# Optimization experiments

Hardware: AMD Instinct MI355X
Metric: run time of the kernel (lower is better)

Reference implementation:

```python
import jax, jax.numpy as jnp
import numpy as np
import math

SHAPES = [(64, 64), (32, 32), (16, 16), (8, 8)]  # (H_l, W_l), sum HW = 5440
N, LQ, D, NH, NL, NP = 4, 5440, 256, 8, 4, 4
HD = D // NH


def _offset_bias():
    thetas = np.arange(NH, dtype=np.float64) * (2.0 * math.pi / NH)
    grid = np.stack([np.cos(thetas), np.sin(thetas)], -1)
    grid = grid / np.abs(grid).max(-1, keepdims=True)
    grid = np.tile(grid[:, None, None, :], (1, NL, NP, 1))
    grid = grid * (np.arange(NP) + 1)[None, None, :, None]
    return jnp.asarray(grid.reshape(-1), jnp.float32)


def setup_inputs() -> dict:
    key = jax.random.key(0)
    ks = jax.random.split(key, 16)
    s = 1.0 / math.sqrt(D)
    inp = {
        'query0': jax.random.normal(ks[0], (N, LQ, D), jnp.float32),
        'query1': jax.random.normal(ks[1], (N, LQ, D), jnp.float32),
        'feat0': jax.random.normal(ks[2], (N, LQ, D), jnp.float32),
        'feat1': jax.random.normal(ks[3], (N, LQ, D), jnp.float32),
        'reference_points': jax.random.uniform(ks[4], (N, LQ, NL, 2), jnp.float32),
        'W_off': 0.01 * jax.random.normal(ks[5], (NH * NL * NP * 2, D), jnp.float32),
        'b_off': _offset_bias(),
        'W_attn': 0.01 * jax.random.normal(ks[6], (NH * NL * NP, D), jnp.float32),
        'b_attn': jnp.zeros((NH * NL * NP,), jnp.float32),
        'W_val': s * jax.random.normal(ks[7], (D, D), jnp.float32),
        'b_val': jnp.zeros((D,), jnp.float32),
        'W_out': s * jax.random.normal(ks[8], (D, D), jnp.float32),
        'b_out': jnp.zeros((D,), jnp.float32),
        'W_agg': s * jax.random.normal(ks[9], (D, 2 * D), jnp.float32),
        'b_agg': jnp.zeros((D,), jnp.float32),
    }
    return inp


def _sample_level(value_l, H, W, loc):
    # value_l: (N, H*W, NH, HD); loc: (N, LQ, NH, NP, 2) normalized in [0,1]
    v_t = value_l.transpose(0, 2, 1, 3)  # (N, NH, HW, HD)
    # grid_sample bilinear, align_corners=False, zero padding:
    x = loc[..., 0] * W - 0.5
    y = loc[..., 1] * H - 0.5
    x0 = jnp.floor(x); y0 = jnp.floor(y)
    lx = x - x0; ly = y - y0
    x0 = x0.astype(jnp.int32); y0 = y0.astype(jnp.int32)

    def corner(xi, yi, w):
        valid = (xi >= 0) & (xi < W) & (yi >= 0) & (yi < H)
        flat = jnp.clip(yi, 0, H - 1) * W + jnp.clip(xi, 0, W - 1)  # (N,LQ,NH,NP)
        ft = flat.transpose(0, 2, 1, 3).reshape(flat.shape[0], flat.shape[2], -1)
        g = jnp.take_along_axis(v_t, ft[..., None], axis=2)  # (N,NH,LQ*NP,HD)
        g = g.reshape(v_t.shape[0], v_t.shape[1], loc.shape[1], loc.shape[3], -1)
        g = g.transpose(0, 2, 1, 3, 4)  # (N,LQ,NH,NP,HD)
        return g * (w * valid)[..., None]

    return (corner(x0, y0, (1 - lx) * (1 - ly)) + corner(x0 + 1, y0, lx * (1 - ly))
            + corner(x0, y0 + 1, (1 - lx) * ly) + corner(x0 + 1, y0 + 1, lx * ly))


def reference(query0, query1, feat0, feat1, reference_points, W_off, b_off,
              W_attn, b_attn, W_val, b_val, W_out, b_out, W_agg, b_agg):
    offset_norm = jnp.asarray([[w, h] for (h, w) in SHAPES], jnp.float32)  # (NL, 2)
    sizes = [h * w for h, w in SHAPES]
    splits = list(np.cumsum(sizes)[:-1])
    outs = []
    for q, feat in ((query0, feat0), (query1, feat1)):
        value = (feat @ W_val.T + b_val).reshape(N, -1, NH, HD)
        off = (q @ W_off.T + b_off).reshape(N, LQ, NH, NL, NP, 2)
        attn = (q @ W_attn.T + b_attn).reshape(N, LQ, NH, NL * NP)
        attn = jax.nn.softmax(attn, axis=-1).reshape(N, LQ, NH, NL, NP)
        loc = reference_points[:, :, None, :, None, :] + off / offset_norm[None, None, None, :, None, :]
        vals = jnp.split(value, splits, axis=1)
        acc = jnp.zeros((N, LQ, NH, HD), value.dtype)
        for l, (H, W) in enumerate(SHAPES):
            s = _sample_level(vals[l], H, W, loc[:, :, :, l])  # (N,LQ,NH,NP,HD)
            acc = acc + jnp.einsum('nqhpd,nqhp->nqhd', s, attn[:, :, :, l])
        outs.append(acc.reshape(N, LQ, D) @ W_out.T + b_out)
    return jnp.concatenate(outs, axis=-1) @ W_agg.T + b_agg
```

## Files before the change

### kernel.cpp

```cpp
#include <hip/hip_runtime.h>
#include <math.h>

#define N_   4
#define LQ_  5440
#define MQ_  (N_*LQ_)

typedef _Float16 f16;
typedef __attribute__((ext_vector_type(2))) _Float16 f16x2;
typedef __attribute__((ext_vector_type(8))) _Float16 f16x8;
typedef __attribute__((ext_vector_type(4))) float     f32x4;

__device__ __forceinline__ unsigned short f2h(float f) {
  union { f16 h; unsigned short u; } v; v.h = (f16)f; return v.u;
}
__device__ __forceinline__ float h2f(unsigned u) {
  union { unsigned short u; f16 h; } v; v.u = (unsigned short)u; return (float)v.h;
}
__device__ __forceinline__ f16x2 u2h2(unsigned u) {
  union { unsigned u; f16x2 h; } v; v.u = u; return v.h;
}

#define GLD16(gp, lp) __builtin_amdgcn_global_load_lds( \
    (const __attribute__((address_space(1))) void*)(gp), \
    (__attribute__((address_space(3))) void*)(lp), 16, 0, 0)

__global__ __launch_bounds__(256)
void prep(const float* __restrict__ W_val, const float* __restrict__ W_off,
          const float* __restrict__ W_attn, const float* __restrict__ W_agg,
          const float* __restrict__ W_out, const float* __restrict__ b_off,
          const float* __restrict__ b_attn, const float* __restrict__ b_agg,
          const float* __restrict__ b_out,
          unsigned short* __restrict__ Wvalh, unsigned short* __restrict__ Wcath,
          unsigned short* __restrict__ Wfinh, float* __restrict__ bcat,
          float* __restrict__ bfin) {
  __shared__ float wrow[256];
  const int b = blockIdx.x, t = threadIdx.x;
  if (b < 160) {
    const float* src; unsigned short* dst; int i;
    if (b < 64)       { src = W_val;  dst = Wvalh;          i = b * 256 + t; }
    else if (b < 128) { src = W_off;  dst = Wcath;          i = (b - 64) * 256 + t; }
    else              { src = W_attn; dst = Wcath + 65536;  i = (b - 128) * 256 + t; }
    float4 v = reinterpret_cast<const float4*>(src)[i];
    ushort4 r;
    r.x = f2h(v.x); r.y = f2h(v.y); r.z = f2h(v.z); r.w = f2h(v.w);
    reinterpret_cast<ushort4*>(dst)[i] = r;
  } else if (b < 672) {
    const int idx = b - 160, j = idx & 255, s = idx >> 8;
    wrow[t] = W_agg[(size_t)j * 512 + s * 256 + t];
    __syncthreads();
    float a = 0.f;
    for (int i = 0; i < 256; ++i) a = fmaf(wrow[i], W_out[(size_t)i * 256 + t], a);
    Wfinh[(size_t)j * 512 + s * 256 + t] = f2h(a);
  } else if (b == 672) {
    float s = b_agg[t];
    for (int i = 0; i < 256; ++i)
      s = fmaf(W_agg[(size_t)t * 512 + i] + W_agg[(size_t)t * 512 + 256 + i], b_out[i], s);
    bfin[t] = s;
  } else if (b == 673) {
    bcat[t] = b_off[t];
  } else {
    if (t < 128) bcat[256 + t] = b_attn[t];
  }
}

__global__ __launch_bounds__(256)
void gemm_stage1(const float* __restrict__ q0, const float* __restrict__ q1,
                 const float* __restrict__ f0, const float* __restrict__ f1,
                 const unsigned short* __restrict__ Wvalh,
                 const unsigned short* __restrict__ Wcath,
                 const float* __restrict__ b_val, const float* __restrict__ bcat,
                 unsigned short* __restrict__ valb, unsigned short* __restrict__ oab) {
  __shared__ __align__(16) unsigned short As[128 * 64];
  __shared__ __align__(16) unsigned short Ws[128 * 64];
  const int src = blockIdx.y, z = blockIdx.z;
  const size_t SZ = (size_t)MQ_ * 256;
  const float* A; const unsigned short* W; const float* bias;
  unsigned short* C; int NC, NT;
  if (src == 0) { A = z ? f1 : f0; W = Wvalh; bias = b_val; C = valb + z * SZ;               NC = 256; NT = 2; }
  else          { A = z ? q1 : q0; W = Wcath; bias = bcat;  C = oab + (size_t)z * MQ_ * 384; NC = 384; NT = 3; }

  const int t    = threadIdx.x;
  const int lane = t & 63;
  const int wv   = t >> 6;
  const int wr   = wv >> 1, wc = wv & 1;
  const int row0 = blockIdx.x * 128;
  const int srow = t >> 3, schunk = t & 7;
  const int wbase = wv * 512;

  for (int ct = 0; ct < NT; ++ct) {
    const int col0 = ct * 128;
    f32x4 acc[4][4] = {};

    for (int k0 = 0; k0 < 256; k0 += 64) {
      __syncthreads();
      #pragma unroll
      for (int i = 0; i < 4; ++i) {
        const int row = i * 32 + srow;
        const int ch  = schunk ^ (row & 7);
        GLD16(W + (size_t)(col0 + row) * 256 + k0 + ch * 8, &Ws[i * 2048 + wbase]);
      }
      #pragma unroll
      for (int i = 0; i < 4; ++i) {
        const int row = i * 32 + srow;
        const float* srcp = A + (size_t)(row0 + row) * 256 + k0 + schunk * 8;
        const float4 a0 = *reinterpret_cast<const float4*>(srcp);
        const float4 a1 = *reinterpret_cast<const float4*>(srcp + 4);
        f16x8 hv;
        hv[0] = (f16)a0.x; hv[1] = (f16)a0.y; hv[2] = (f16)a0.z; hv[3] = (f16)a0.w;
        hv[4] = (f16)a1.x; hv[5] = (f16)a1.y; hv[6] = (f16)a1.z; hv[7] = (f16)a1.w;
        const int ch = schunk ^ (row & 7);
        *reinterpret_cast<f16x8*>(&As[row * 64 + ch * 8]) = hv;
      }
      __syncthreads();

      f16x8 af[4][2], bfr[4][2];
      #pragma unroll
      for (int f = 0; f < 4; ++f)
        #pragma unroll
        for (int kk = 0; kk < 2; ++kk) {
          const int ra = wr * 64 + f * 16 + (lane & 15);
          const int ca = (kk * 4 + (lane >> 4)) ^ (ra & 7);
          af[f][kk] = *(const f16x8*)&As[ra * 64 + ca * 8];
          const int rb = wc * 64 + f * 16 + (lane & 15);
          const int cb = (kk * 4 + (lane >> 4)) ^ (rb & 7);
          bfr[f][kk] = *(const f16x8*)&Ws[rb * 64 + cb * 8];
        }
      #pragma unroll
      for (int kk = 0; kk < 2; ++kk)
        #pragma unroll
        for (int fm = 0; fm < 4; ++fm)
          #pragma unroll
          for (int fn = 0; fn < 4; ++fn)
            acc[fm][fn] = __builtin_amdgcn_mfma_f32_16x16x32_f16(
                af[fm][kk], bfr[fn][kk], acc[fm][fn], 0, 0, 0);
    }

    #pragma unroll
    for (int fm = 0; fm < 4; ++fm) {
      const int m = row0 + wr * 64 + fm * 16 + (lane >> 4) * 4;
      #pragma unroll
      for (int fn = 0; fn < 4; ++fn) {
        const int c = col0 + wc * 64 + fn * 16 + (lane & 15);
        const float bv = bias[c];
        #pragma unroll
        for (int r = 0; r < 4; ++r)
          C[(size_t)(m + r) * NC + c] = f2h(acc[fm][fn][r] + bv);
      }
    }
  }
}

__global__ __launch_bounds__(256)
void gemm_final(const unsigned short* __restrict__ A,
                const unsigned short* __restrict__ W,
                const float* __restrict__ bias, float* __restrict__ out) {
  __shared__ __align__(16) unsigned short As[64 * 64];
  __shared__ __align__(16) unsigned short Ws[128 * 64];
  const int t    = threadIdx.x;
  const int lane = t & 63;
  const int wv   = t >> 6;
  const int row0 = blockIdx.x * 64, col0 = blockIdx.y * 128;
  const int srow = t >> 3, schunk = t & 7;
  const int wbase = wv * 512;

  f32x4 acc[4][2] = {};

  for (int k0 = 0; k0 < 512; k0 += 64) {
    __syncthreads();
    #pragma unroll
    for (int i = 0; i < 2; ++i) {
      const int row = i * 32 + srow;
      const int ch  = schunk ^ (row & 7);
      GLD16(A + (size_t)(row0 + row) * 512 + k0 + ch * 8, &As[i * 2048 + wbase]);
    }
    #pragma unroll
    for (int i = 0; i < 4; ++i) {
      const int row = i * 32 + srow;
      const int ch  = schunk ^ (row & 7);
      GLD16(W + (size_t)(col0 + row) * 512 + k0 + ch * 8, &Ws[i * 2048 + wbase]);
    }
    __syncthreads();

    f16x8 af[4][2], bfr[2][2];
    #pragma unroll
    for (int kk = 0; kk < 2; ++kk) {
      #pragma unroll
      for (int f = 0; f < 4; ++f) {
        const int ra = f * 16 + (lane & 15);
        const int ca = (kk * 4 + (lane >> 4)) ^ (ra & 7);
        af[f][kk] = *(const f16x8*)&As[ra * 64 + ca * 8];
      }
      #pragma unroll
      for (int fn = 0; fn < 2; ++fn) {
        const int rb = wv * 32 + fn * 16 + (lane & 15);
        const int cb = (kk * 4 + (lane >> 4)) ^ (rb & 7);
        bfr[fn][kk] = *(const f16x8*)&Ws[rb * 64 + cb * 8];
      }
    }
    #pragma unroll
    for (int kk = 0; kk < 2; ++kk)
      #pragma unroll
      for (int fm = 0; fm < 4; ++fm)
        #pragma unroll
        for (int fn = 0; fn < 2; ++fn)
          acc[fm][fn] = __builtin_amdgcn_mfma_f32_16x16x32_f16(
              af[fm][kk], bfr[fn][kk], acc[fm][fn], 0, 0, 0);
  }

  #pragma unroll
  for (int fm = 0; fm < 4; ++fm) {
    const int m = row0 + fm * 16 + (lane >> 4) * 4;
    #pragma unroll
    for (int fn = 0; fn < 2; ++fn) {
      const int c = col0 + wv * 32 + fn * 16 + (lane & 15);
      const float bv = bias[c];
      #pragma unroll
      for (int r = 0; r < 4; ++r)
        out[(size_t)(m + r) * 256 + c] = acc[fm][fn][r] + bv;
    }
  }
}

__global__ __launch_bounds__(256, 4)
void deform_sample(const unsigned short* __restrict__ vals,
                   const unsigned short* __restrict__ oa,
                   const float* __restrict__ refp,
                   unsigned short* __restrict__ acc_out) {
  const int bid = blockIdx.x;
  const int sn  = bid & 7;
  const int s   = sn >> 2, n = sn & 3;
  const int qb  = bid >> 3;
  const int t   = threadIdx.x;
  const int q   = t >> 5, tq = t & 31;
  const int row = n * LQ_ + qb * 8 + q;
  const int h   = tq >> 2;
  __shared__ uint4 lds_rec[8][16][8];

  const unsigned short* oar = oa + ((size_t)s * MQ_ + row) * 384;
  {
    const int   l  = tq & 3;
    const int   Wn = 64 >> l;
    const float Wf = (float)Wn;
    const int   lb = (int)(((0xAD200u >> (5 * l)) & 31u) << 8);
    const uint4 ov = *reinterpret_cast<const uint4*>(oar + (size_t)tq * 8);
    const uint2 lv = *reinterpret_cast<const uint2*>(oar + 256 + (size_t)tq * 4);
    const float2 rxy = *reinterpret_cast<const float2*>(refp + (size_t)row * 8 + l * 2);
    float lg[4] = { h2f(lv.x), h2f(lv.x >> 16), h2f(lv.y), h2f(lv.y >> 16) };
    float mx = fmaxf(fmaxf(lg[0], lg[1]), fmaxf(lg[2], lg[3]));
    mx = fmaxf(mx, __shfl_xor(mx, 1));
    mx = fmaxf(mx, __shfl_xor(mx, 2));
    float e[4], se;
    #pragma unroll
    for (int k = 0; k < 4; ++k) e[k] = __expf(lg[k] - mx);
    se = (e[0] + e[1]) + (e[2] + e[3]);
    se += __shfl_xor(se, 1);
    se += __shfl_xor(se, 2);
    const float inv = 1.f / se;
    const unsigned od[4] = { ov.x, ov.y, ov.z, ov.w };
    #pragma unroll
    for (int k = 0; k < 4; ++k) {
      const float ox = h2f(od[k]), oy = h2f(od[k] >> 16);
      const float x = fmaf(rxy.x, Wf, ox) - 0.5f;
      const float y = fmaf(rxy.y, Wf, oy) - 0.5f;
      const float x0f = floorf(x), y0f = floorf(y);
      const int   x0 = (int)x0f,   y0 = (int)y0f;
      const float lx = x - x0f,    ly = y - y0f;
      const float aw = e[k] * inv;
      const int   xs[2] = {x0, x0 + 1}, ys[2] = {y0, y0 + 1};
      const float wx[2] = {1.f - lx, lx}, wy[2] = {1.f - ly, ly};
      unsigned ia[4]; unsigned short wa[4];
      #pragma unroll
      for (int cy = 0; cy < 2; ++cy)
        #pragma unroll
        for (int cx = 0; cx < 2; ++cx) {
          const int xi = xs[cx], yi = ys[cy];
          const bool v = (xi >= 0) && (xi < Wn) && (yi >= 0) && (yi < Wn);
          const int xc = min(max(xi, 0), Wn - 1), yc = min(max(yi, 0), Wn - 1);
          ia[cy * 2 + cx] = (unsigned)(lb + yc * Wn + xc);
          wa[cy * 2 + cx] = f2h(v ? wx[cx] * wy[cy] * aw : 0.f);
        }
      const int jj = l * 4 + k;
      uint4 rec;
      rec.x = ia[0] | (ia[1] << 16);
      rec.y = ia[2] | (ia[3] << 16);
      rec.z = (unsigned)wa[0] | ((unsigned)wa[1] << 16);
      rec.w = (unsigned)wa[2] | ((unsigned)wa[3] << 16);
      lds_rec[q][jj][h ^ (jj & 7)] = rec;
    }
  }
  __syncthreads();

  const int dg = tq & 3;
  const char* vb = (const char*)(vals + ((size_t)s * N_ + n) * LQ_ * 256);
  const unsigned hd = (unsigned)((h * 32 + dg * 8) * 2);
  float facc[8] = {};
  #pragma unroll 1
  for (int l4 = 0; l4 < 4; ++l4) {
    uint4 m[4];
    #pragma unroll
    for (int p = 0; p < 4; ++p) {
      const int j = l4 * 4 + p;
      m[p] = lds_rec[q][j][h ^ (j & 7)];
    }
    f16x8 v[16];
    #pragma unroll
    for (int p = 0; p < 4; ++p) {
      v[p * 4 + 0] = *reinterpret_cast<const f16x8*>(vb + (((m[p].x & 0xffffu) << 9) + hd));
      v[p * 4 + 1] = *reinterpret_cast<const f16x8*>(vb + (((m[p].x >> 16) << 9) + hd));
      v[p * 4 + 2] = *reinterpret_cast<const f16x8*>(vb + (((m[p].y & 0xffffu) << 9) + hd));
      v[p * 4 + 3] = *reinterpret_cast<const f16x8*>(vb + (((m[p].y >> 16) << 9) + hd));
    }
    __builtin_amdgcn_sched_barrier(0);
    f16x2 a0 = {0, 0}, a1 = {0, 0}, a2 = {0, 0}, a3 = {0, 0};
    #pragma unroll
    for (int p = 0; p < 4; ++p) {
      const f16x2 w0 = u2h2(__builtin_amdgcn_perm(m[p].z, m[p].z, 0x01000100u));
      const f16x2 w1 = u2h2(__builtin_amdgcn_perm(m[p].z, m[p].z, 0x03020302u));
      const f16x2 w2 = u2h2(__builtin_amdgcn_perm(m[p].w, m[p].w, 0x01000100u));
      const f16x2 w3 = u2h2(__builtin_amdgcn_perm(m[p].w, m[p].w, 0x03020302u));
      const f16x2* p0 = (const f16x2*)&v[p * 4 + 0];
      const f16x2* p1 = (const f16x2*)&v[p * 4 + 1];
      const f16x2* p2 = (const f16x2*)&v[p * 4 + 2];
      const f16x2* p3 = (const f16x2*)&v[p * 4 + 3];
      a0 = __builtin_elementwise_fma(p0[0], w0, a0);
      a1 = __builtin_elementwise_fma(p0[1], w0, a1);
      a2 = __builtin_elementwise_fma(p0[2], w0, a2);
      a3 = __builtin_elementwise_fma(p0[3], w0, a3);
      a0 = __builtin_elementwise_fma(p1[0], w1, a0);
      a1 = __builtin_elementwise_fma(p1[1], w1, a1);
      a2 = __builtin_elementwise_fma(p1[2], w1, a2);
      a3 = __builtin_elementwise_fma(p1[3], w1, a3);
      a0 = __builtin_elementwise_fma(p2[0], w2, a0);
      a1 = __builtin_elementwise_fma(p2[1], w2, a1);
      a2 = __builtin_elementwise_fma(p2[2], w2, a2);
      a3 = __builtin_elementwise_fma(p2[3], w2, a3);
      a0 = __builtin_elementwise_fma(p3[0], w3, a0);
      a1 = __builtin_elementwise_fma(p3[1], w3, a1);
      a2 = __builtin_elementwise_fma(p3[2], w3, a2);
      a3 = __builtin_elementwise_fma(p3[3], w3, a3);
    }
    facc[0] += (float)a0[0]; facc[1] += (float)a0[1];
    facc[2] += (float)a1[0]; facc[3] += (float)a1[1];
    facc[4] += (float)a2[0]; facc[5] += (float)a2[1];
    facc[6] += (float)a3[0]; facc[7] += (float)a3[1];
  }
  f16x8 r;
  #pragma unroll
  for (int e2 = 0; e2 < 8; ++e2) r[e2] = (f16)facc[e2];
  *reinterpret_cast<f16x8*>(acc_out + (size_t)row * 512 + s * 256 + h * 32 + dg * 8) = r;
}

extern "C" void kernel_launch(void* const* d_in, const int* in_sizes, int n_in,
                              void* d_out, int out_size, void* d_ws, size_t ws_size,
                              hipStream_t stream) {
  const float* query0 = (const float*)d_in[0];
  const float* query1 = (const float*)d_in[1];
  const float* feat0  = (const float*)d_in[2];
  const float* feat1  = (const float*)d_in[3];
  const float* refp   = (const float*)d_in[4];
  const float* W_off  = (const float*)d_in[5];
  const float* b_off  = (const float*)d_in[6];
  const float* W_attn = (const float*)d_in[7];
  const float* b_attn = (const float*)d_in[8];
  const float* W_val  = (const float*)d_in[9];
  const float* b_val  = (const float*)d_in[10];
  const float* W_out  = (const float*)d_in[11];
  const float* b_out  = (const float*)d_in[12];
  const float* W_agg  = (const float*)d_in[13];
  const float* b_agg  = (const float*)d_in[14];
  float* out = (float*)d_out;

  char* p = (char*)d_ws;
  const size_t SZ = (size_t)MQ_ * 256;
  unsigned short* valb  = (unsigned short*)p; p += 2 * SZ * 2;
  unsigned short* oab   = (unsigned short*)p; p += (size_t)2 * MQ_ * 384 * 2;
  unsigned short* accb  = (unsigned short*)p; p += (size_t)MQ_ * 512 * 2;
  unsigned short* Wvalh = (unsigned short*)p; p += 256 * 256 * 2;
  unsigned short* Wcath = (unsigned short*)p; p += 384 * 256 * 2;
  unsigned short* Wfinh = (unsigned short*)p; p += 256 * 512 * 2;
  float* bcat = (float*)p; p += 384 * 4;
  float* bfin = (float*)p; p += 256 * 4;

  prep<<<675, 256, 0, stream>>>(W_val, W_off, W_attn, W_agg, W_out, b_off, b_attn,
                                b_agg, b_out, Wvalh, Wcath, Wfinh, bcat, bfin);
  gemm_stage1<<<dim3(170, 2, 2), 256, 0, stream>>>(query0, query1, feat0, feat1,
                                                   Wvalh, Wcath, b_val, bcat,
                                                   valb, oab);
  deform_sample<<<5440, 256, 0, stream>>>(valb, oab, refp, accb);
  gemm_final<<<dim3(340, 2), 256, 0, stream>>>(accb, Wfinh, bfin, out);
}
```

Baseline: 137.1 us.

## Remove prep kernel by converting weights inline and folding W_out into sampler

The separate prep launch goes away. gemm_stage1 now reads the fp32 W_val, W_off and W_attn directly and converts them to fp16 while staging into LDS, replacing the async global_load_lds copy of pre-converted weights, and it reads the bias arrays directly. The W_agg·W_out fusion and the final bias computation become 513 extra blocks appended to the deform_sample grid, which removes one kernel launch and its serialization gap. In exchange, the GEMM does redundant fp32 weight loads and conversions in every block, and the extra tail blocks in the sampler are compute-serial.

```diff
diff --git a/kernel.cpp b/kernel.cpp
--- a/kernel.cpp
+++ b/kernel.cpp
@@ -25,59 +25,20 @@
     (__attribute__((address_space(3))) void*)(lp), 16, 0, 0)
 
 __global__ __launch_bounds__(256)
-void prep(const float* __restrict__ W_val, const float* __restrict__ W_off,
-          const float* __restrict__ W_attn, const float* __restrict__ W_agg,
-          const float* __restrict__ W_out, const float* __restrict__ b_off,
-          const float* __restrict__ b_attn, const float* __restrict__ b_agg,
-          const float* __restrict__ b_out,
-          unsigned short* __restrict__ Wvalh, unsigned short* __restrict__ Wcath,
-          unsigned short* __restrict__ Wfinh, float* __restrict__ bcat,
-          float* __restrict__ bfin) {
-  __shared__ float wrow[256];
-  const int b = blockIdx.x, t = threadIdx.x;
-  if (b < 160) {
-    const float* src; unsigned short* dst; int i;
-    if (b < 64)       { src = W_val;  dst = Wvalh;          i = b * 256 + t; }
-    else if (b < 128) { src = W_off;  dst = Wcath;          i = (b - 64) * 256 + t; }
-    else              { src = W_attn; dst = Wcath + 65536;  i = (b - 128) * 256 + t; }
-    float4 v = reinterpret_cast<const float4*>(src)[i];
-    ushort4 r;
-    r.x = f2h(v.x); r.y = f2h(v.y); r.z = f2h(v.z); r.w = f2h(v.w);
-    reinterpret_cast<ushort4*>(dst)[i] = r;
-  } else if (b < 672) {
-    const int idx = b - 160, j = idx & 255, s = idx >> 8;
-    wrow[t] = W_agg[(size_t)j * 512 + s * 256 + t];
-    __syncthreads();
-    float a = 0.f;
-    for (int i = 0; i < 256; ++i) a = fmaf(wrow[i], W_out[(size_t)i * 256 + t], a);
-    Wfinh[(size_t)j * 512 + s * 256 + t] = f2h(a);
-  } else if (b == 672) {
-    float s = b_agg[t];
-    for (int i = 0; i < 256; ++i)
-      s = fmaf(W_agg[(size_t)t * 512 + i] + W_agg[(size_t)t * 512 + 256 + i], b_out[i], s);
-    bfin[t] = s;
-  } else if (b == 673) {
-    bcat[t] = b_off[t];
-  } else {
-    if (t < 128) bcat[256 + t] = b_attn[t];
-  }
-}
-
-__global__ __launch_bounds__(256)
 void gemm_stage1(const float* __restrict__ q0, const float* __restrict__ q1,
                  const float* __restrict__ f0, const float* __restrict__ f1,
-                 const unsigned short* __restrict__ Wvalh,
-                 const unsigned short* __restrict__ Wcath,
-                 const float* __restrict__ b_val, const float* __restrict__ bcat,
+                 const float* __restrict__ Wval32, const float* __restrict__ Woff32,
+                 const float* __restrict__ Wattn32,
+                 const float* __restrict__ b_val, const float* __restrict__ b_off,
+                 const float* __restrict__ b_attn,
                  unsigned short* __restrict__ valb, unsigned short* __restrict__ oab) {
   __shared__ __align__(16) unsigned short As[128 * 64];
   __shared__ __align__(16) unsigned short Ws[128 * 64];
   const int src = blockIdx.y, z = blockIdx.z;
   const size_t SZ = (size_t)MQ_ * 256;
-  const float* A; const unsigned short* W; const float* bias;
-  unsigned short* C; int NC, NT;
-  if (src == 0) { A = z ? f1 : f0; W = Wvalh; bias = b_val; C = valb + z * SZ;               NC = 256; NT = 2; }
-  else          { A = z ? q1 : q0; W = Wcath; bias = bcat;  C = oab + (size_t)z * MQ_ * 384; NC = 384; NT = 3; }
+  const float* A; unsigned short* C; int NC, NT;
+  if (src == 0) { A = z ? f1 : f0; C = valb + z * SZ;               NC = 256; NT = 2; }
+  else          { A = z ? q1 : q0; C = oab + (size_t)z * MQ_ * 384; NC = 384; NT = 3; }
 
   const int t    = threadIdx.x;
   const int lane = t & 63;
@@ -85,10 +46,14 @@
   const int wr   = wv >> 1, wc = wv & 1;
   const int row0 = blockIdx.x * 128;
   const int srow = t >> 3, schunk = t & 7;
-  const int wbase = wv * 512;
 
   for (int ct = 0; ct < NT; ++ct) {
     const int col0 = ct * 128;
+    const float* Wsrc; const float* bias; int wrow0;
+    if (src == 0)      { Wsrc = Wval32;  bias = b_val  + col0; wrow0 = col0; }
+    else if (ct < 2)   { Wsrc = Woff32;  bias = b_off  + col0; wrow0 = col0; }
+    else               { Wsrc = Wattn32; bias = b_attn;        wrow0 = 0;    }
+
     f32x4 acc[4][4] = {};
 
     for (int k0 = 0; k0 < 256; k0 += 64) {
@@ -96,8 +61,14 @@
       #pragma unroll
       for (int i = 0; i < 4; ++i) {
         const int row = i * 32 + srow;
-        const int ch  = schunk ^ (row & 7);
-        GLD16(W + (size_t)(col0 + row) * 256 + k0 + ch * 8, &Ws[i * 2048 + wbase]);
+        const float* wp = Wsrc + (size_t)(wrow0 + row) * 256 + k0 + schunk * 8;
+        const float4 w0 = *reinterpret_cast<const float4*>(wp);
+        const float4 w1 = *reinterpret_cast<const float4*>(wp + 4);
+        f16x8 hw;
+        hw[0] = (f16)w0.x; hw[1] = (f16)w0.y; hw[2] = (f16)w0.z; hw[3] = (f16)w0.w;
+        hw[4] = (f16)w1.x; hw[5] = (f16)w1.y; hw[6] = (f16)w1.z; hw[7] = (f16)w1.w;
+        const int ch = schunk ^ (row & 7);
+        *reinterpret_cast<f16x8*>(&Ws[row * 64 + ch * 8]) = hw;
       }
       #pragma unroll
       for (int i = 0; i < 4; ++i) {
@@ -140,11 +111,11 @@
       const int m = row0 + wr * 64 + fm * 16 + (lane >> 4) * 4;
       #pragma unroll
       for (int fn = 0; fn < 4; ++fn) {
-        const int c = col0 + wc * 64 + fn * 16 + (lane & 15);
-        const float bv = bias[c];
+        const int cl = wc * 64 + fn * 16 + (lane & 15);
+        const float bv = bias[cl];
         #pragma unroll
         for (int r = 0; r < 4; ++r)
-          C[(size_t)(m + r) * NC + c] = f2h(acc[fm][fn][r] + bv);
+          C[(size_t)(m + r) * NC + col0 + cl] = f2h(acc[fm][fn][r] + bv);
       }
     }
   }
@@ -225,16 +196,41 @@
 void deform_sample(const unsigned short* __restrict__ vals,
                    const unsigned short* __restrict__ oa,
                    const float* __restrict__ refp,
-                   unsigned short* __restrict__ acc_out) {
+                   unsigned short* __restrict__ acc_out,
+                   const float* __restrict__ W_agg, const float* __restrict__ W_out,
+                   const float* __restrict__ b_agg, const float* __restrict__ b_out,
+                   unsigned short* __restrict__ Wfinh, float* __restrict__ bfin) {
+  __shared__ uint4 lds_rec[8][16][8];
   const int bid = blockIdx.x;
+  const int t   = threadIdx.x;
+
+  if (bid >= 5440) {
+    const int pb = bid - 5440;
+    float* wrow = (float*)lds_rec;
+    if (pb < 512) {
+      const int j = pb & 255, s2 = pb >> 8;
+      wrow[t] = W_agg[(size_t)j * 512 + s2 * 256 + t];
+      __syncthreads();
+      float a = 0.f;
+      for (int i = 0; i < 256; ++i)
+        a = fmaf(wrow[i], W_out[(size_t)i * 256 + t], a);
+      Wfinh[(size_t)j * 512 + s2 * 256 + t] = f2h(a);
+    } else {
+      float s2 = b_agg[t];
+      for (int i = 0; i < 256; ++i)
+        s2 = fmaf(W_agg[(size_t)t * 512 + i] + W_agg[(size_t)t * 512 + 256 + i],
+                  b_out[i], s2);
+      bfin[t] = s2;
+    }
+    return;
+  }
+
   const int sn  = bid & 7;
   const int s   = sn >> 2, n = sn & 3;
   const int qb  = bid >> 3;
-  const int t   = threadIdx.x;
   const int q   = t >> 5, tq = t & 31;
   const int row = n * LQ_ + qb * 8 + q;
   const int h   = tq >> 2;
-  __shared__ uint4 lds_rec[8][16][8];
 
   const unsigned short* oar = oa + ((size_t)s * MQ_ + row) * 384;
   {
@@ -375,17 +371,15 @@
   unsigned short* valb  = (unsigned short*)p; p += 2 * SZ * 2;
   unsigned short* oab   = (unsigned short*)p; p += (size_t)2 * MQ_ * 384 * 2;
   unsigned short* accb  = (unsigned short*)p; p += (size_t)MQ_ * 512 * 2;
-  unsigned short* Wvalh = (unsigned short*)p; p += 256 * 256 * 2;
-  unsigned short* Wcath = (unsigned short*)p; p += 384 * 256 * 2;
   unsigned short* Wfinh = (unsigned short*)p; p += 256 * 512 * 2;
-  float* bcat = (float*)p; p += 384 * 4;
   float* bfin = (float*)p; p += 256 * 4;
 
-  prep<<<675, 256, 0, stream>>>(W_val, W_off, W_attn, W_agg, W_out, b_off, b_attn,
-                                b_agg, b_out, Wvalh, Wcath, Wfinh, bcat, bfin);
   gemm_stage1<<<dim3(170, 2, 2), 256, 0, stream>>>(query0, query1, feat0, feat1,
-                                                   Wvalh, Wcath, b_val, bcat,
+                                                   W_val, W_off, W_attn,
+                                                   b_val, b_off, b_attn,
                                                    valb, oab);
-  deform_sample<<<5440, 256, 0, stream>>>(valb, oab, refp, accb);
+  deform_sample<<<5440 + 513, 256, 0, stream>>>(valb, oab, refp, accb,
+                                                W_agg, W_out, b_agg, b_out,
+                                                Wfinh, bfin);
   gemm_final<<<dim3(340, 2), 256, 0, stream>>>(accb, Wfinh, bfin, out);
 }
```

Measured after the change: 155.8 us. 13.6% more time.
